# Optimization experiments

Measured on AMD Instinct MI355X. Metric: run time of the kernel, lower is better.

## Reference

```python
import math
import jax, jax.numpy as jnp
import numpy as np

C, H, R, PD = 256, 6, 32, 16
HEAD_SCALE = 1.0 / math.sqrt(R)


def setup_inputs() -> dict:
    key = jax.random.key(0)
    ks = jax.random.split(key, 8)
    B, Lp1 = 8, 4097
    feats = jax.random.normal(ks[0], (B, Lp1, C), dtype=jnp.float32)
    # params (stored [in, out] for x @ W)
    Wq = jax.random.normal(ks[1], (C, H * R), dtype=jnp.float32) / math.sqrt(C)
    Wk = jax.random.normal(ks[2], (C, H * R), dtype=jnp.float32) / math.sqrt(C)
    Wpi = jax.random.normal(ks[3], (C, PD), dtype=jnp.float32) / math.sqrt(C)
    bpi = jnp.zeros((PD,), jnp.float32)
    Wpj = jax.random.normal(ks[4], (C, PD), dtype=jnp.float32) / math.sqrt(C)
    bpj = jnp.zeros((PD,), jnp.float32)
    Wd = jax.random.normal(ks[5], (C, 1), dtype=jnp.float32) / math.sqrt(C)
    bd = jnp.zeros((1,), jnp.float32)
    alpha_pair = jnp.float32(0.5)
    logit_scale = jnp.float32(1.0)
    return {"feats": feats, "Wq": Wq, "Wk": Wk, "Wpi": Wpi, "bpi": bpi,
            "Wpj": Wpj, "bpj": bpj, "Wd": Wd, "bd": bd,
            "alpha_pair": alpha_pair, "logit_scale": logit_scale}


def _fold_vertices(feats):
    x = feats[:, 1:]                      # drop first token
    B, L, Cc = x.shape
    return x.reshape(B, L // 2, 2, Cc).mean(axis=2)  # [B, N, C]


def reference(feats, Wq, Wk, Wpi, bpi, Wpj, bpj, Wd, bd, alpha_pair, logit_scale):
    x = _fold_vertices(feats)             # [B, N, C]
    B, N, _ = x.shape
    Q = (x @ Wq).reshape(B, N, H, R)
    K = (x @ Wk).reshape(B, N, H, R)
    # sum over heads fused into one contraction (math-equal to per-head scores summed)
    S = jnp.einsum('bnhr,bmhr->bnm', Q, K) * HEAD_SCALE   # [B, N, N]
    a_i = jax.nn.relu(x @ Wpi + bpi)      # [B, N, PD]
    b_j = jax.nn.relu(x @ Wpj + bpj)
    S = S + jnp.maximum(alpha_pair, 0.0) * jnp.einsum('bnd,bmd->bnm', a_i, b_j)
    d = (x @ Wd + bd)[..., 0]             # [B, N]
    idx = jnp.arange(N)
    S = S.at[:, idx, idx].add(d)
    return S * jnp.maximum(logit_scale, 0.01)
```

## Files before the change

### kernel.cpp

```cpp
#include <hip/hip_runtime.h>
#include <hip/hip_bf16.h>
#include <stdint.h>

typedef __attribute__((ext_vector_type(8))) short short8;
typedef __attribute__((ext_vector_type(4))) short short4v;
typedef __attribute__((ext_vector_type(4))) float f32x4;
typedef __attribute__((ext_vector_type(4))) unsigned uint4v;

#define NB 8
#define NN 2048
#define CC 256
#define LP1 4097
#define HR 192
#define PDim 16
#define KP 224
#define NPAD 448
#define HEAD_SCALE 0.17677669529663689f

#define GLOAD16(g, l) __builtin_amdgcn_global_load_lds( \
    (const __attribute__((address_space(1))) unsigned int*)(g), \
    (__attribute__((address_space(3))) unsigned int*)(l), 16, 0, 0)

static __device__ __forceinline__ unsigned short bf16bits(float f) {
    __hip_bfloat16 h = __float2bfloat16(f);
    return *(unsigned short*)&h;
}

__global__ __launch_bounds__(256) void k0_prep(
    const float* __restrict__ Wq, const float* __restrict__ Wk,
    const float* __restrict__ Wpi, const float* __restrict__ Wpj,
    const float* __restrict__ Wd,
    __hip_bfloat16* __restrict__ WT,
    unsigned* __restrict__ Ppad, unsigned* __restrict__ Rpad)
{
    const int WTN = NPAD*CC;
    const int PV  = NB*NN*2;
    int i = blockIdx.x*blockDim.x + threadIdx.x;
    if (i < WTN) {
        int c = i >> 8, k = i & 255;
        float v;
        if (c < HR)                 v = Wq[k*HR + c] * HEAD_SCALE;
        else if (c < 2*HR)          v = Wk[k*HR + (c-HR)];
        else if (c < 2*HR+PDim)     v = Wpi[k*PDim + (c-2*HR)];
        else if (c < 2*HR+2*PDim)   v = Wpj[k*PDim + (c-2*HR-PDim)];
        else if (c == 416)          v = Wd[k];
        else                        v = 0.f;
        WT[i] = __float2bfloat16(v);
    } else {
        int j = i - WTN;
        unsigned* arr = (j < PV) ? Ppad : Rpad;
        int q = (j < PV) ? j : j - PV;
        int row = q >> 1, of = 104 + (q & 1)*4;
        *(uint4v*)(arr + (size_t)row*(KP/2) + of) = (uint4v){0,0,0,0};
    }
}

__global__ __launch_bounds__(256, 3) void ka_proj(
    const float* __restrict__ feats, const __hip_bfloat16* __restrict__ WT,
    const float* __restrict__ bpi, const float* __restrict__ bpj,
    const float* __restrict__ bd, const float* __restrict__ alpha_pair,
    __hip_bfloat16* __restrict__ P, __hip_bfloat16* __restrict__ R,
    float* __restrict__ dvec)
{
    __shared__ __hip_bfloat16 lds[32*256];

    int t = threadIdx.x;
    int lane = t & 63;
    int w = t >> 6;
    int l15 = lane & 15, lg = lane >> 4;
    int row0 = blockIdx.x * 32;
    int b = row0 >> 11;
    int n0loc = row0 & (NN-1);

    {
        int r = t >> 3, cg = t & 7;
        size_t fb = ((size_t)b*LP1 + 1 + 2*(size_t)(n0loc + r))*CC + cg*32;
#pragma unroll
        for (int s = 0; s < 4; ++s) {
            float4 a0 = *(const float4*)(feats + fb + s*8);
            float4 a1 = *(const float4*)(feats + fb + s*8 + 4);
            float4 c0 = *(const float4*)(feats + fb + CC + s*8);
            float4 c1 = *(const float4*)(feats + fb + CC + s*8 + 4);
            unsigned short h[8];
            h[0] = bf16bits(0.5f*(a0.x + c0.x));
            h[1] = bf16bits(0.5f*(a0.y + c0.y));
            h[2] = bf16bits(0.5f*(a0.z + c0.z));
            h[3] = bf16bits(0.5f*(a0.w + c0.w));
            h[4] = bf16bits(0.5f*(a1.x + c1.x));
            h[5] = bf16bits(0.5f*(a1.y + c1.y));
            h[6] = bf16bits(0.5f*(a1.z + c1.z));
            h[7] = bf16bits(0.5f*(a1.w + c1.w));
            int slot = (cg*4 + s) ^ (r & 7);
            *(short8*)((char*)lds + r*512 + slot*16) = *(const short8*)h;
        }
    }
    __syncthreads();

    const __hip_bfloat16* pB[7];
#pragma unroll
    for (int ni = 0; ni < 7; ++ni)
        pB[ni] = WT + (size_t)(w*112 + ni*16 + l15)*CC + lg*8;

    f32x4 acc[7][2];
#pragma unroll
    for (int ni = 0; ni < 7; ++ni)
#pragma unroll
        for (int mi = 0; mi < 2; ++mi)
            acc[ni][mi] = (f32x4){0.f, 0.f, 0.f, 0.f};

    int arow[2];
#pragma unroll
    for (int mi = 0; mi < 2; ++mi) arow[mi] = (mi*16 + l15)*512;
    int rx = l15 & 7;

#pragma unroll
    for (int kk = 0; kk < 8; ++kk) {
        short8 a[2], bb[7];
        int slotb = ((kk*4 + lg) ^ rx) << 4;
#pragma unroll
        for (int mi = 0; mi < 2; ++mi)
            a[mi] = *(const short8*)((const char*)lds + arow[mi] + slotb);
#pragma unroll
        for (int ni = 0; ni < 7; ++ni) bb[ni] = *(const short8*)(pB[ni] + kk*32);
#pragma unroll
        for (int ni = 0; ni < 7; ++ni)
#pragma unroll
            for (int mi = 0; mi < 2; ++mi)
                acc[ni][mi] = __builtin_amdgcn_mfma_f32_16x16x32_bf16(
                    bb[ni], a[mi], acc[ni][mi], 0, 0, 0);
    }

    float alpha_eff = fmaxf(alpha_pair[0], 0.f);
    float bd0 = bd[0];
#pragma unroll
    for (int ni = 0; ni < 7; ++ni) {
        int cb = w*112 + ni*16 + lg*4;
#pragma unroll
        for (int mi = 0; mi < 2; ++mi) {
            int n = n0loc + mi*16 + l15;
            size_t rb = ((size_t)b*NN + n)*KP;
            f32x4 v = acc[ni][mi];
            if (cb < HR) {
                short4v h;
#pragma unroll
                for (int j = 0; j < 4; ++j) h[j] = (short)bf16bits(v[j]);
                *(short4v*)(P + rb + cb) = h;
            } else if (cb < 2*HR) {
                short4v h;
#pragma unroll
                for (int j = 0; j < 4; ++j) h[j] = (short)bf16bits(v[j]);
                *(short4v*)(R + rb + (cb - HR)) = h;
            } else if (cb < 2*HR + PDim) {
                int pc = cb - 2*HR;
                short4v h;
#pragma unroll
                for (int j = 0; j < 4; ++j)
                    h[j] = (short)bf16bits(fmaxf(v[j] + bpi[pc+j], 0.f) * alpha_eff);
                *(short4v*)(P + rb + HR + pc) = h;
            } else if (cb < 2*HR + 2*PDim) {
                int pc = cb - 2*HR - PDim;
                short4v h;
#pragma unroll
                for (int j = 0; j < 4; ++j)
                    h[j] = (short)bf16bits(fmaxf(v[j] + bpj[pc+j], 0.f));
                *(short4v*)(R + rb + HR + pc) = h;
            } else if (cb == 416) {
                dvec[(size_t)b*NN + n] = v[0] + bd0;
            }
        }
    }
}

__global__ __launch_bounds__(256, 4) void kb_pair(
    const __hip_bfloat16* __restrict__ P, const __hip_bfloat16* __restrict__ R,
    const float* __restrict__ dvec, const float* __restrict__ logit_scale,
    float* __restrict__ out)
{
    __shared__ __hip_bfloat16 ldsA[2][128*32];
    __shared__ __hip_bfloat16 ldsB[2][128*32];

    int t = threadIdx.x;
    int lane = t & 63;
    int w = t >> 6;
    int wr = w >> 1, wc = w & 1;
    int l15 = lane & 15, lg = lane >> 4;

    int hw = blockIdx.x;
    int b = hw & 7;
    int within = hw >> 3;
    int m0 = (within & 15) << 7;
    int n0 = (within >> 4) << 7;

    const char* srcA[2];
    const char* srcB[2];
#pragma unroll
    for (int i = 0; i < 2; ++i) {
        int row   = i*64 + (t >> 2);
        int scolb = ((t & 3) << 4) ^ ((row & 3) << 4);
        srcA[i] = (const char*)(P + ((size_t)b*NN + n0 + row)*KP) + scolb;
        srcB[i] = (const char*)(R + ((size_t)b*NN + m0 + row)*KP) + scolb;
    }
    int ldst = w * 1024;

    int abyte = (wr*64 + l15)*64 + ((lg ^ (l15 & 3)) << 4);
    int bbyte = (wc*64 + l15)*64 + ((lg ^ (l15 & 3)) << 4);

    f32x4 acc[4][4];
#pragma unroll
    for (int ni = 0; ni < 4; ++ni)
#pragma unroll
        for (int mi = 0; mi < 4; ++mi)
            acc[ni][mi] = (f32x4){0.f, 0.f, 0.f, 0.f};

#pragma unroll
    for (int i = 0; i < 2; ++i) {
        GLOAD16(srcA[i], (char*)(&ldsA[0][0]) + i*4096 + ldst);
        GLOAD16(srcB[i], (char*)(&ldsB[0][0]) + i*4096 + ldst);
    }

    int buf = 0;
#pragma unroll
    for (int s = 0; s < 7; ++s) {
        __syncthreads();
        if (s < 6) {
            size_t kof = (size_t)(s + 1) * 64;
#pragma unroll
            for (int i = 0; i < 2; ++i) {
                GLOAD16(srcA[i] + kof, (char*)(&ldsA[buf ^ 1][0]) + i*4096 + ldst);
                GLOAD16(srcB[i] + kof, (char*)(&ldsB[buf ^ 1][0]) + i*4096 + ldst);
            }
        }
        short8 a[4], bb[4];
#pragma unroll
        for (int mi = 0; mi < 4; ++mi)
            a[mi] = *(const short8*)((const char*)(&ldsA[buf][0]) + abyte + mi*1024);
#pragma unroll
        for (int ni = 0; ni < 4; ++ni)
            bb[ni] = *(const short8*)((const char*)(&ldsB[buf][0]) + bbyte + ni*1024);
#pragma unroll
        for (int ni = 0; ni < 4; ++ni)
#pragma unroll
            for (int mi = 0; mi < 4; ++mi)
                acc[ni][mi] = __builtin_amdgcn_mfma_f32_16x16x32_bf16(
                    bb[ni], a[mi], acc[ni][mi], 0, 0, 0);
        buf ^= 1;
    }

    float ls = fmaxf(logit_scale[0], 0.01f);
    bool diag_tile = (n0 == m0);
#pragma unroll
    for (int ni = 0; ni < 4; ++ni) {
#pragma unroll
        for (int mi = 0; mi < 4; ++mi) {
            int orow  = n0 + wr*64 + mi*16 + l15;
            int cbase = m0 + wc*64 + ni*16 + lg*4;
            f32x4 v = acc[ni][mi];
            if (diag_tile) {
                int dj = orow - cbase;
                if (dj >= 0 && dj < 4) v[dj] += dvec[(size_t)b*NN + orow];
            }
            f32x4 o;
#pragma unroll
            for (int j = 0; j < 4; ++j) o[j] = v[j] * ls;
            *(f32x4*)(out + ((size_t)b*NN + orow)*NN + cbase) = o;
        }
    }
}

extern "C" void kernel_launch(void* const* d_in, const int* in_sizes, int n_in,
                              void* d_out, int out_size, void* d_ws, size_t ws_size,
                              hipStream_t stream)
{
    const float* feats = (const float*)d_in[0];
    const float* Wq    = (const float*)d_in[1];
    const float* Wk    = (const float*)d_in[2];
    const float* Wpi   = (const float*)d_in[3];
    const float* bpi   = (const float*)d_in[4];
    const float* Wpj   = (const float*)d_in[5];
    const float* bpj   = (const float*)d_in[6];
    const float* Wd    = (const float*)d_in[7];
    const float* bd    = (const float*)d_in[8];
    const float* alpha = (const float*)d_in[9];
    const float* lsc   = (const float*)d_in[10];

    char* ws = (char*)d_ws;
    __hip_bfloat16* WT = (__hip_bfloat16*)(ws);
    __hip_bfloat16* P  = (__hip_bfloat16*)(ws + 229376);
    __hip_bfloat16* R  = (__hip_bfloat16*)(ws + 7569408);
    float*          dv = (float*)(ws + 14909440);

    k0_prep<<<704, 256, 0, stream>>>(Wq, Wk, Wpi, Wpj, Wd,
                                     WT, (unsigned*)P, (unsigned*)R);
    ka_proj<<<512, 256, 0, stream>>>(feats, WT, bpi, bpj, bd, alpha, P, R, dv);
    kb_pair<<<2048, 256, 0, stream>>>(P, R, dv, lsc, (float*)d_out);
}
```

Baseline: 69.94 us.

## Widen pair-score tile to 128x256 with 8 waves; halve projection block rows

The pair-score kernel now uses 512-thread blocks that each compute a 128x256 output tile. The P tile is shared across twice as many columns, which cuts redundant global and LDS loads of the projected operands. The diagonal-tile check is adjusted to match the new tile shape. The projection kernel now handles 16 rows per block instead of 32, doubling the grid with smaller per-block register and LDS footprints and a higher occupancy target. Larger blocks in the pair kernel may lower occupancy and reduce the number of blocks available to balance across CUs.

```diff
diff --git a/kernel.cpp b/kernel.cpp
--- a/kernel.cpp
+++ b/kernel.cpp
@@ -55,28 +55,28 @@
     }
 }
 
-__global__ __launch_bounds__(256, 3) void ka_proj(
+__global__ __launch_bounds__(256, 4) void ka_proj(
     const float* __restrict__ feats, const __hip_bfloat16* __restrict__ WT,
     const float* __restrict__ bpi, const float* __restrict__ bpj,
     const float* __restrict__ bd, const float* __restrict__ alpha_pair,
     __hip_bfloat16* __restrict__ P, __hip_bfloat16* __restrict__ R,
     float* __restrict__ dvec)
 {
-    __shared__ __hip_bfloat16 lds[32*256];
+    __shared__ __hip_bfloat16 lds[16*256];
 
     int t = threadIdx.x;
     int lane = t & 63;
     int w = t >> 6;
     int l15 = lane & 15, lg = lane >> 4;
-    int row0 = blockIdx.x * 32;
+    int row0 = blockIdx.x * 16;
     int b = row0 >> 11;
     int n0loc = row0 & (NN-1);
 
     {
-        int r = t >> 3, cg = t & 7;
-        size_t fb = ((size_t)b*LP1 + 1 + 2*(size_t)(n0loc + r))*CC + cg*32;
-#pragma unroll
-        for (int s = 0; s < 4; ++s) {
+        int r = t >> 4, cg = t & 15;
+        size_t fb = ((size_t)b*LP1 + 1 + 2*(size_t)(n0loc + r))*CC + cg*16;
+#pragma unroll
+        for (int s = 0; s < 2; ++s) {
             float4 a0 = *(const float4*)(feats + fb + s*8);
             float4 a1 = *(const float4*)(feats + fb + s*8 + 4);
             float4 c0 = *(const float4*)(feats + fb + CC + s*8);
@@ -90,7 +90,7 @@
             h[5] = bf16bits(0.5f*(a1.y + c1.y));
             h[6] = bf16bits(0.5f*(a1.z + c1.z));
             h[7] = bf16bits(0.5f*(a1.w + c1.w));
-            int slot = (cg*4 + s) ^ (r & 7);
+            int slot = (cg*2 + s) ^ (r & 7);
             *(short8*)((char*)lds + r*512 + slot*16) = *(const short8*)h;
         }
     }
@@ -101,105 +101,98 @@
     for (int ni = 0; ni < 7; ++ni)
         pB[ni] = WT + (size_t)(w*112 + ni*16 + l15)*CC + lg*8;
 
-    f32x4 acc[7][2];
-#pragma unroll
-    for (int ni = 0; ni < 7; ++ni)
-#pragma unroll
-        for (int mi = 0; mi < 2; ++mi)
-            acc[ni][mi] = (f32x4){0.f, 0.f, 0.f, 0.f};
-
-    int arow[2];
-#pragma unroll
-    for (int mi = 0; mi < 2; ++mi) arow[mi] = (mi*16 + l15)*512;
+    f32x4 acc[7];
+#pragma unroll
+    for (int ni = 0; ni < 7; ++ni) acc[ni] = (f32x4){0.f, 0.f, 0.f, 0.f};
+
+    int arow = l15*512;
     int rx = l15 & 7;
 
 #pragma unroll
     for (int kk = 0; kk < 8; ++kk) {
-        short8 a[2], bb[7];
-        int slotb = ((kk*4 + lg) ^ rx) << 4;
-#pragma unroll
-        for (int mi = 0; mi < 2; ++mi)
-            a[mi] = *(const short8*)((const char*)lds + arow[mi] + slotb);
+        short8 a = *(const short8*)((const char*)lds + arow + ((((kk*4+lg) ^ rx)) << 4));
+        short8 bb[7];
 #pragma unroll
         for (int ni = 0; ni < 7; ++ni) bb[ni] = *(const short8*)(pB[ni] + kk*32);
 #pragma unroll
         for (int ni = 0; ni < 7; ++ni)
-#pragma unroll
-            for (int mi = 0; mi < 2; ++mi)
-                acc[ni][mi] = __builtin_amdgcn_mfma_f32_16x16x32_bf16(
-                    bb[ni], a[mi], acc[ni][mi], 0, 0, 0);
+            acc[ni] = __builtin_amdgcn_mfma_f32_16x16x32_bf16(
+                bb[ni], a, acc[ni], 0, 0, 0);
     }
 
     float alpha_eff = fmaxf(alpha_pair[0], 0.f);
     float bd0 = bd[0];
+    int n = n0loc + l15;
+    size_t rb = ((size_t)b*NN + n)*KP;
 #pragma unroll
     for (int ni = 0; ni < 7; ++ni) {
         int cb = w*112 + ni*16 + lg*4;
-#pragma unroll
-        for (int mi = 0; mi < 2; ++mi) {
-            int n = n0loc + mi*16 + l15;
-            size_t rb = ((size_t)b*NN + n)*KP;
-            f32x4 v = acc[ni][mi];
-            if (cb < HR) {
-                short4v h;
-#pragma unroll
-                for (int j = 0; j < 4; ++j) h[j] = (short)bf16bits(v[j]);
-                *(short4v*)(P + rb + cb) = h;
-            } else if (cb < 2*HR) {
-                short4v h;
-#pragma unroll
-                for (int j = 0; j < 4; ++j) h[j] = (short)bf16bits(v[j]);
-                *(short4v*)(R + rb + (cb - HR)) = h;
-            } else if (cb < 2*HR + PDim) {
-                int pc = cb - 2*HR;
-                short4v h;
-#pragma unroll
-                for (int j = 0; j < 4; ++j)
-                    h[j] = (short)bf16bits(fmaxf(v[j] + bpi[pc+j], 0.f) * alpha_eff);
-                *(short4v*)(P + rb + HR + pc) = h;
-            } else if (cb < 2*HR + 2*PDim) {
-                int pc = cb - 2*HR - PDim;
-                short4v h;
-#pragma unroll
-                for (int j = 0; j < 4; ++j)
-                    h[j] = (short)bf16bits(fmaxf(v[j] + bpj[pc+j], 0.f));
-                *(short4v*)(R + rb + HR + pc) = h;
-            } else if (cb == 416) {
-                dvec[(size_t)b*NN + n] = v[0] + bd0;
-            }
-        }
-    }
-}
-
-__global__ __launch_bounds__(256, 4) void kb_pair(
+        f32x4 v = acc[ni];
+        if (cb < HR) {
+            short4v h;
+#pragma unroll
+            for (int j = 0; j < 4; ++j) h[j] = (short)bf16bits(v[j]);
+            *(short4v*)(P + rb + cb) = h;
+        } else if (cb < 2*HR) {
+            short4v h;
+#pragma unroll
+            for (int j = 0; j < 4; ++j) h[j] = (short)bf16bits(v[j]);
+            *(short4v*)(R + rb + (cb - HR)) = h;
+        } else if (cb < 2*HR + PDim) {
+            int pc = cb - 2*HR;
+            short4v h;
+#pragma unroll
+            for (int j = 0; j < 4; ++j)
+                h[j] = (short)bf16bits(fmaxf(v[j] + bpi[pc+j], 0.f) * alpha_eff);
+            *(short4v*)(P + rb + HR + pc) = h;
+        } else if (cb < 2*HR + 2*PDim) {
+            int pc = cb - 2*HR - PDim;
+            short4v h;
+#pragma unroll
+            for (int j = 0; j < 4; ++j)
+                h[j] = (short)bf16bits(fmaxf(v[j] + bpj[pc+j], 0.f));
+            *(short4v*)(R + rb + HR + pc) = h;
+        } else if (cb == 416) {
+            dvec[(size_t)b*NN + n] = v[0] + bd0;
+        }
+    }
+}
+
+__global__ __launch_bounds__(512, 4) void kb_pair(
     const __hip_bfloat16* __restrict__ P, const __hip_bfloat16* __restrict__ R,
     const float* __restrict__ dvec, const float* __restrict__ logit_scale,
     float* __restrict__ out)
 {
     __shared__ __hip_bfloat16 ldsA[2][128*32];
-    __shared__ __hip_bfloat16 ldsB[2][128*32];
+    __shared__ __hip_bfloat16 ldsB[2][256*32];
 
     int t = threadIdx.x;
     int lane = t & 63;
     int w = t >> 6;
-    int wr = w >> 1, wc = w & 1;
+    int wr = w >> 2, wc = w & 3;
     int l15 = lane & 15, lg = lane >> 4;
 
     int hw = blockIdx.x;
     int b = hw & 7;
     int within = hw >> 3;
-    int m0 = (within & 15) << 7;
-    int n0 = (within >> 4) << 7;
-
-    const char* srcA[2];
+    int n0 = (within & 15) << 7;
+    int m0 = (within >> 4) << 8;
+
+    const char* srcA;
     const char* srcB[2];
-#pragma unroll
-    for (int i = 0; i < 2; ++i) {
-        int row   = i*64 + (t >> 2);
-        int scolb = ((t & 3) << 4) ^ ((row & 3) << 4);
-        srcA[i] = (const char*)(P + ((size_t)b*NN + n0 + row)*KP) + scolb;
-        srcB[i] = (const char*)(R + ((size_t)b*NN + m0 + row)*KP) + scolb;
-    }
+    {
+        int rowA = t >> 2;
+        int scA = ((t & 3) << 4) ^ ((rowA & 3) << 4);
+        srcA = (const char*)(P + ((size_t)b*NN + n0 + rowA)*KP) + scA;
+#pragma unroll
+        for (int i = 0; i < 2; ++i) {
+            int rowB = i*128 + (t >> 2);
+            int scB = ((t & 3) << 4) ^ ((rowB & 3) << 4);
+            srcB[i] = (const char*)(R + ((size_t)b*NN + m0 + rowB)*KP) + scB;
+        }
+    }
+    char* A0 = (char*)&ldsA[0][0];
+    char* B0 = (char*)&ldsB[0][0];
     int ldst = w * 1024;
 
     int abyte = (wr*64 + l15)*64 + ((lg ^ (l15 & 3)) << 4);
@@ -212,11 +205,9 @@
         for (int mi = 0; mi < 4; ++mi)
             acc[ni][mi] = (f32x4){0.f, 0.f, 0.f, 0.f};
 
-#pragma unroll
-    for (int i = 0; i < 2; ++i) {
-        GLOAD16(srcA[i], (char*)(&ldsA[0][0]) + i*4096 + ldst);
-        GLOAD16(srcB[i], (char*)(&ldsB[0][0]) + i*4096 + ldst);
-    }
+    GLOAD16(srcA,    A0 + ldst);
+    GLOAD16(srcB[0], B0 + ldst);
+    GLOAD16(srcB[1], B0 + 8192 + ldst);
 
     int buf = 0;
 #pragma unroll
@@ -224,19 +215,17 @@
         __syncthreads();
         if (s < 6) {
             size_t kof = (size_t)(s + 1) * 64;
-#pragma unroll
-            for (int i = 0; i < 2; ++i) {
-                GLOAD16(srcA[i] + kof, (char*)(&ldsA[buf ^ 1][0]) + i*4096 + ldst);
-                GLOAD16(srcB[i] + kof, (char*)(&ldsB[buf ^ 1][0]) + i*4096 + ldst);
-            }
+            GLOAD16(srcA + kof,    A0 + (buf^1)*8192 + ldst);
+            GLOAD16(srcB[0] + kof, B0 + (buf^1)*16384 + ldst);
+            GLOAD16(srcB[1] + kof, B0 + (buf^1)*16384 + 8192 + ldst);
         }
         short8 a[4], bb[4];
 #pragma unroll
         for (int mi = 0; mi < 4; ++mi)
-            a[mi] = *(const short8*)((const char*)(&ldsA[buf][0]) + abyte + mi*1024);
+            a[mi] = *(const short8*)(A0 + buf*8192 + abyte + mi*1024);
 #pragma unroll
         for (int ni = 0; ni < 4; ++ni)
-            bb[ni] = *(const short8*)((const char*)(&ldsB[buf][0]) + bbyte + ni*1024);
+            bb[ni] = *(const short8*)(B0 + buf*16384 + bbyte + ni*1024);
 #pragma unroll
         for (int ni = 0; ni < 4; ++ni)
 #pragma unroll
@@ -247,7 +236,7 @@
     }
 
     float ls = fmaxf(logit_scale[0], 0.01f);
-    bool diag_tile = (n0 == m0);
+    bool diag_tile = ((n0 >> 8) == (m0 >> 8));
 #pragma unroll
     for (int ni = 0; ni < 4; ++ni) {
 #pragma unroll
@@ -291,6 +280,6 @@
 
     k0_prep<<<704, 256, 0, stream>>>(Wq, Wk, Wpi, Wpj, Wd,
                                      WT, (unsigned*)P, (unsigned*)R);
-    ka_proj<<<512, 256, 0, stream>>>(feats, WT, bpi, bpj, bd, alpha, P, R, dv);
-    kb_pair<<<2048, 256, 0, stream>>>(P, R, dv, lsc, (float*)d_out);
-}
+    ka_proj<<<1024, 256, 0, stream>>>(feats, WT, bpi, bpj, bd, alpha, P, R, dv);
+    kb_pair<<<1024, 512, 0, stream>>>(P, R, dv, lsc, (float*)d_out);
+}
```

Result: slower. 80.89 us (+15.7%).
